# Kernel tuning notes

Measured on AMD Instinct MI355X. Metric: run time of the kernel, lower is better.

## Reference

```python
import jax, jax.numpy as jnp
import numpy as np

B, S, D = 4, 4096, 1024
GROUP = 256
HEAD = 128
INNER = 2048


def setup_inputs() -> dict:
    key = jax.random.key(0)
    ks = jax.random.split(key, 16)
    s = 0.02
    return {
        'x': jax.random.normal(ks[0], (B, S, D), jnp.float32),
        'Wv': jax.random.normal(ks[1], (D, INNER), jnp.float32) * s,
        'bv': jnp.zeros((INNER,), jnp.float32),
        'Wg': jax.random.normal(ks[2], (D, INNER), jnp.float32) * s,
        'bg': jnp.zeros((INNER,), jnp.float32),
        'Win': jax.random.normal(ks[3], (D, HEAD), jnp.float32) * s,
        'bin_': jnp.zeros((HEAD,), jnp.float32),
        'Wout': jax.random.normal(ks[4], (INNER, D), jnp.float32) * s,
        'bout': jnp.zeros((D,), jnp.float32),
        'g_qq': 1.0 + jax.random.normal(ks[5], (HEAD,), jnp.float32) * s,
        'b_qq': jnp.zeros((HEAD,), jnp.float32),
        'g_qk': 1.0 + jax.random.normal(ks[6], (HEAD,), jnp.float32) * s,
        'b_qk': jnp.zeros((HEAD,), jnp.float32),
        'g_lq': 1.0 + jax.random.normal(ks[7], (HEAD,), jnp.float32) * s,
        'b_lq': jnp.zeros((HEAD,), jnp.float32),
        'g_lk': 1.0 + jax.random.normal(ks[8], (HEAD,), jnp.float32) * s,
        'b_lk': jnp.zeros((HEAD,), jnp.float32),
    }


def reference(x, Wv, bv, Wg, bg, Win, bin_, Wout, bout,
              g_qq, b_qq, g_qk, b_qk, g_lq, b_lq, g_lk, b_lk):
    b, s, d = x.shape
    g = s // GROUP
    xc = x.reshape(b, g, GROUP, d)                       # [B,G,C,D]
    v = jax.nn.silu(xc @ Wv + bv)                        # [B,G,C,E]
    gate = jax.nn.silu(xc @ Wg + bg)                     # [B,G,C,E]
    x_ = jax.nn.silu(xc @ Win + bin_)                    # [B,G,C,H]
    quad_q = x_ * g_qq + b_qq
    quad_k = x_ * g_qk + b_qk
    lin_q = x_ * g_lq + b_lq
    lin_k = x_ * g_lk + b_lk
    # local quadratic relu^2 attention per chunk
    scale = jnp.asarray(INNER ** 0.5, x.dtype)           # v.size(-1)**0.5
    attn = jnp.einsum('bgns,bgms->bgnm', quad_q, quad_k) / scale
    causal_mask = jnp.triu(jnp.ones((GROUP, GROUP), bool), 1)
    attn = jnp.where(causal_mask, 0.0, attn)
    attn = jnp.square(jax.nn.relu(attn))
    v_quad = jnp.einsum('bgnm,bgme->bgne', attn, v)
    # global causal linear attention: exclusive cumsum of per-chunk k^T v over chunks
    kv = jnp.einsum('bgcs,bgce->bgse', lin_k, v)         # [B,G,H,E]
    kv = jnp.cumsum(kv, axis=1) - kv                     # exclusive over chunk dim
    v_lin = jnp.einsum('bgcs,bgse->bgce', lin_q, kv)
    o = (v_quad + v_lin) * gate
    o = o @ Wout + bout
    return o.reshape(b, s, d)
```

## Files before the change

kernel.cpp:

```cpp
#include <hip/hip_runtime.h>

typedef __attribute__((ext_vector_type(8))) short short8;
typedef __attribute__((ext_vector_type(4))) float floatx4;
typedef __attribute__((ext_vector_type(4))) unsigned short ushort4v;
typedef unsigned short u16;

#define DEV __device__ __forceinline__

DEV u16 f2bf(float f) {
  unsigned int u = __float_as_uint(f);
  u += 0x7fffu + ((u >> 16) & 1u);
  return (u16)(u >> 16);
}
DEV float bf2f(u16 h) { return __uint_as_float(((unsigned int)h) << 16); }
DEV float silu_f(float x) { return x / (1.f + __expf(-x)); }
DEV floatx4 fzero() { floatx4 z = {0.f, 0.f, 0.f, 0.f}; return z; }
DEV floatx4 mfma16(short8 a, short8 b, floatx4 c) {
  return __builtin_amdgcn_mfma_f32_16x16x32_bf16(a, b, c, 0, 0, 0);
}
DEV void gll16(const void* g, void* l) {
  __builtin_amdgcn_global_load_lds((__attribute__((address_space(1))) void*)g,
                                   (__attribute__((address_space(3))) void*)l,
                                   16, 0, 0);
}

__global__ __launch_bounds__(256) void cast_x_kernel(const float* __restrict__ x,
                                                     u16* __restrict__ xb, int n4) {
  int i = blockIdx.x * 256 + threadIdx.x;
  if (i >= n4) return;
  float4 v = ((const float4*)x)[i];
  ushort4v o;
  o[0] = f2bf(v.x); o[1] = f2bf(v.y); o[2] = f2bf(v.z); o[3] = f2bf(v.w);
  *(ushort4v*)&xb[(size_t)i * 4] = o;
}

__global__ __launch_bounds__(256) void transpose_cast_kernel(const float* __restrict__ W,
                                                             u16* __restrict__ WT,
                                                             int K, int N) {
  __shared__ u16 tile[32][36];
  int n0 = blockIdx.x * 32, k0 = blockIdx.y * 32;
  int t = threadIdx.x;
  int r = t >> 3, cs = (t & 7) * 4;
  float4 v = *(const float4*)&W[(size_t)(k0 + r) * N + n0 + cs];
  tile[r][cs + 0] = f2bf(v.x);
  tile[r][cs + 1] = f2bf(v.y);
  tile[r][cs + 2] = f2bf(v.z);
  tile[r][cs + 3] = f2bf(v.w);
  __syncthreads();
  ushort4v o;
  o[0] = tile[cs + 0][r];
  o[1] = tile[cs + 1][r];
  o[2] = tile[cs + 2][r];
  o[3] = tile[cs + 3][r];
  *(ushort4v*)&WT[(size_t)(n0 + r) * K + k0 + cs] = o;
}

DEV void wave_transposed_store(u16* __restrict__ Ct, long chunk_stride,
                               const u16* trw, int chunk, int cbase, int nbase,
                               int lane) {
#pragma unroll
  for (int it = 0; it < 8; ++it) {
    int e_l = it * 8 + (lane >> 3);
    int c_off = (lane & 7) * 8;
    short8 val = *(const short8*)&trw[e_l * 72 + c_off];
    *(short8*)&Ct[(size_t)chunk * chunk_stride + (size_t)(nbase + e_l) * 256 + cbase +
                  c_off] = val;
  }
}


#define PH(SA, SB, NIA, NIB, VML, RDA, STG, HH)                                \
  {                                                                            \
    asm volatile("s_waitcnt vmcnt(" #VML ")" ::: "memory");                    \
    if (RDA) {                                                                 \
      _Pragma("unroll") for (int mi_ = 0; mi_ < 8; ++mi_)                      \
          af[mi_] = *(const short8*)&lds[((SA) * 1024 + aoff + mi_ * 64) * 8]; \
    }                                                                          \
    bf0 = *(const short8*)&lds[((SB) * 1024 + boff + (NIA) * 64) * 8];         \
    bf1 = *(const short8*)&lds[((SB) * 1024 + boff + (NIB) * 64) * 8];         \
    if (STG) STAGE(HH);                                                        \
    asm volatile("" ::: "memory");                                             \
    __builtin_amdgcn_s_barrier();                                              \
    asm volatile("" ::: "memory");                                             \
    __builtin_amdgcn_s_setprio(1);                                             \
    _Pragma("unroll") for (int mi_ = 0; mi_ < 8; ++mi_) {                      \
      acc[mi_][NIA] = mfma16(af[mi_], bf0, acc[mi_][NIA]);                     \
      acc[mi_][NIB] = mfma16(af[mi_], bf1, acc[mi_][NIB]);                     \
    }                                                                          \
    __builtin_amdgcn_s_setprio(0);                                             \
    asm volatile("" ::: "memory");                                             \
    __builtin_amdgcn_s_barrier();                                              \
    asm volatile("" ::: "memory");                                             \
  }

template <int MODE>
__global__ __launch_bounds__(512, 2) void gemm8(
    const u16* __restrict__ A, const u16* __restrict__ Bt,
    const float* __restrict__ bias0, const float* __restrict__ bias1,
    u16* __restrict__ vT, u16* __restrict__ gate, float* __restrict__ Cf) {
  constexpr int KK = (MODE == 0) ? 1024 : 2048;
  constexpr int NN = (MODE == 0) ? 4096 : 1024;
  constexpr int NT = KK / 64;
  constexpr int NSH = (MODE == 0) ? 4 : 2;

  __shared__ u16 lds[8 * 8192];

  const int t = threadIdx.x;
  const int wave = t >> 6, lane = t & 63;
  const int l15 = lane & 15, l16 = lane >> 4;
  const int b = blockIdx.x;
  const int xcd = b & 7, i = b >> 3;
  const int m0 = (xcd * 8 + (i >> NSH)) * 256;
  const int n0 = (i & ((1 << NSH) - 1)) * 256;
  const int wm = wave >> 2, wn = wave & 3;

  const int o0 = wave * 128 + lane;
  const int r0 = o0 >> 2;
  const int p0 = (o0 & 3) ^ ((r0 >> 1) & 3);
  const u16* srcA = A + (size_t)(m0 + r0) * KK + p0 * 8;
  const u16* srcB = Bt + (size_t)(n0 + r0) * KK + p0 * 8;

  auto STAGE = [&](int h) {
    const int slot = h & 7;
    const int koff = (h >> 2) * 64 + ((h >> 1) & 1) * 32;
    u16* dst = &lds[slot * 8192 + o0 * 8];
    const u16* s = ((h & 1) ? srcB : srcA) + koff;
    gll16(s, dst);
    gll16(s + 16 * KK, dst + 512);
  };

  const int rA = wm * 128 + l15;
  const int aoff = rA * 4 + (l16 ^ ((rA >> 1) & 3));
  const int rB = wn * 64 + l15;
  const int boff = rB * 4 + (l16 ^ ((rB >> 1) & 3));

  floatx4 acc[8][4];
#pragma unroll
  for (int a = 0; a < 8; ++a)
#pragma unroll
    for (int c = 0; c < 4; ++c) acc[a][c] = fzero();
  short8 af[8], bf0, bf1;

#pragma unroll
  for (int h = 0; h < 7; ++h) STAGE(h);
  asm volatile("s_waitcnt vmcnt(10)" ::: "memory");
  asm volatile("" ::: "memory");
  __builtin_amdgcn_s_barrier();
  asm volatile("" ::: "memory");

  for (int T = 0; T < NT - 2; ++T) {
    const int s0 = (T & 1) * 4;
    PH(s0, s0 + 1, 0, 1, 8, 1, 1, 4 * T + 7)
    PH(s0, s0 + 1, 2, 3, 8, 0, 1, 4 * T + 8)
    PH(s0 + 2, s0 + 3, 0, 1, 8, 1, 1, 4 * T + 9)
    PH(s0 + 2, s0 + 3, 2, 3, 8, 0, 1, 4 * T + 10)
  }
  {
    const int s0 = ((NT - 2) & 1) * 4;
    PH(s0, s0 + 1, 0, 1, 8, 1, 1, 4 * (NT - 2) + 7)
    PH(s0, s0 + 1, 2, 3, 8, 0, 0, 0)
    PH(s0 + 2, s0 + 3, 0, 1, 6, 1, 0, 0)
    PH(s0 + 2, s0 + 3, 2, 3, 4, 0, 0, 0)
  }
  {
    const int s0 = ((NT - 1) & 1) * 4;
    PH(s0, s0 + 1, 0, 1, 2, 1, 0, 0)
    PH(s0, s0 + 1, 2, 3, 0, 0, 0, 0)
    PH(s0 + 2, s0 + 3, 0, 1, 0, 1, 0, 0)
    PH(s0 + 2, s0 + 3, 2, 3, 0, 0, 0, 0)
  }

  if constexpr (MODE == 0) {
    const int chunk = m0 >> 8;
    u16* trw = &lds[wave * (64 * 72)];
    if (n0 < 2048) {
      const int e0 = n0 + wn * 64;
#pragma unroll
      for (int th = 0; th < 2; ++th) {
#pragma unroll
        for (int mi2 = 0; mi2 < 4; ++mi2) {
          const int mi = th * 4 + mi2;
#pragma unroll
          for (int ni = 0; ni < 4; ++ni) {
            const float bc = bias0[e0 + ni * 16 + l15];
            ushort4v pk;
#pragma unroll
            for (int r = 0; r < 4; ++r) pk[r] = f2bf(silu_f(acc[mi][ni][r] + bc));
            *(ushort4v*)&trw[(ni * 16 + l15) * 72 + mi2 * 16 + l16 * 4] = pk;
          }
        }
        wave_transposed_store(vT, 2048L * 256, trw, chunk, wm * 128 + th * 64, e0,
                              lane);
      }
    } else {
      const int c0 = n0 - 2048 + wn * 64;
#pragma unroll
      for (int th = 0; th < 2; ++th) {
#pragma unroll
        for (int mi2 = 0; mi2 < 4; ++mi2) {
          const int mi = th * 4 + mi2;
#pragma unroll
          for (int ni = 0; ni < 4; ++ni) {
            const float bc = bias1[c0 + ni * 16 + l15];
#pragma unroll
            for (int r = 0; r < 4; ++r)
              trw[(mi2 * 16 + l16 * 4 + r) * 72 + ni * 16 + l15] =
                  f2bf(silu_f(acc[mi][ni][r] + bc));
          }
        }
#pragma unroll
        for (int it = 0; it < 8; ++it) {
          const int m_l = it * 8 + (lane >> 3);
          const int n_off = (lane & 7) * 8;
          *(short8*)&gate[(size_t)(m0 + wm * 128 + th * 64 + m_l) * 2048 + c0 +
                          n_off] = *(const short8*)&trw[m_l * 72 + n_off];
        }
      }
    }
  } else {
#pragma unroll
    for (int mi = 0; mi < 8; ++mi)
#pragma unroll
      for (int ni = 0; ni < 4; ++ni) {
        const int col = n0 + wn * 64 + ni * 16 + l15;
        const float bc = bias0[col];
        const int row = m0 + wm * 128 + mi * 16 + l16 * 4;
#pragma unroll
        for (int r = 0; r < 4; ++r)
          Cf[(size_t)(row + r) * NN + col] = acc[mi][ni][r] + bc;
      }
  }
}

template <int MODE>
__global__ __launch_bounds__(256) void gemm_bt(
    const u16* __restrict__ A, const u16* __restrict__ Bt, int M, int N, int K,
    int nshift, const float* __restrict__ bias, u16* __restrict__ Cn,
    float* __restrict__ Cf, u16* __restrict__ Ct, long ct_stride,
    u16* __restrict__ Cn2, u16* __restrict__ Cn3,
    const float* __restrict__ gqq, const float* __restrict__ bqq,
    const float* __restrict__ gqk, const float* __restrict__ bqk,
    const float* __restrict__ glq, const float* __restrict__ blq,
    const float* __restrict__ glk, const float* __restrict__ blk) {
  __shared__ union {
    struct { u16 a[128 * 64]; u16 b[128 * 64]; } st;
    u16 tr[4 * 64 * 72];
  } sm;
  const int t = threadIdx.x;
  const int wave = t >> 6, lane = t & 63;
  const int l15 = lane & 15, l16 = lane >> 4;
  const int ell = blockIdx.x;
  const int xcd = ell & 7, i = ell >> 3;
  const int mtiles_per_xcd = M >> 10;
  const int m0 = (xcd * mtiles_per_xcd + (i >> nshift)) * 128;
  const int n0 = (i & ((1 << nshift) - 1)) * 128;
  const int wm = (wave >> 1) * 64, wn = (wave & 1) * 64;

  floatx4 acc[4][4];
#pragma unroll
  for (int i2 = 0; i2 < 4; ++i2)
#pragma unroll
    for (int j = 0; j < 4; ++j) acc[i2][j] = fzero();

  const u16* pa[4];
  const u16* pb[4];
#pragma unroll
  for (int j = 0; j < 4; ++j) {
    const int c = t + 256 * j;
    const int r = c >> 3, p = c & 7;
    const int g = p ^ (r & 7);
    pa[j] = A + (size_t)(m0 + r) * K + g * 8;
    pb[j] = Bt + (size_t)(n0 + r) * K + g * 8;
  }

  for (int k0 = 0; k0 < K; k0 += 64) {
    __syncthreads();
#pragma unroll
    for (int j = 0; j < 4; ++j) {
      gll16(pa[j] + k0, &sm.st.a[(t + 256 * j) * 8]);
      gll16(pb[j] + k0, &sm.st.b[(t + 256 * j) * 8]);
    }
    __syncthreads();
#pragma unroll
    for (int s = 0; s < 2; ++s) {
      short8 af[4], bfr[4];
#pragma unroll
      for (int mi = 0; mi < 4; ++mi) {
        const int wr = wm + mi * 16 + l15;
        af[mi] = *(const short8*)&sm.st.a[wr * 64 + ((s * 4 + l16) ^ (wr & 7)) * 8];
      }
#pragma unroll
      for (int ni = 0; ni < 4; ++ni) {
        const int wr = wn + ni * 16 + l15;
        bfr[ni] = *(const short8*)&sm.st.b[wr * 64 + ((s * 4 + l16) ^ (wr & 7)) * 8];
      }
#pragma unroll
      for (int mi = 0; mi < 4; ++mi)
#pragma unroll
        for (int ni = 0; ni < 4; ++ni)
          acc[mi][ni] = mfma16(af[mi], bfr[ni], acc[mi][ni]);
    }
  }
  __syncthreads();

  if constexpr (MODE == 3) {
#pragma unroll
    for (int mi = 0; mi < 4; ++mi)
#pragma unroll
      for (int ni = 0; ni < 4; ++ni) {
        const int col = n0 + wn + ni * 16 + l15;
        const float bc = bias[col];
        const int row = m0 + wm + mi * 16 + l16 * 4;
#pragma unroll
        for (int r = 0; r < 4; ++r)
          Cf[(size_t)(row + r) * N + col] = acc[mi][ni][r] + bc;
      }
  } else {
    u16* trw = &sm.tr[wave * 64 * 72];
#pragma unroll
    for (int mi = 0; mi < 4; ++mi)
#pragma unroll
      for (int ni = 0; ni < 4; ++ni) {
        const int col = wn + ni * 16 + l15;
        const float bc = bias[col];
        const float Gqq = gqq[col], Bqq = bqq[col];
        const float Gqk = gqk[col], Bqk = bqk[col];
        const float Glq = glq[col], Blq = blq[col];
        const float Glk = glk[col], Blk = blk[col];
        const int row = m0 + wm + mi * 16 + l16 * 4;
        ushort4v p;
#pragma unroll
        for (int r = 0; r < 4; ++r) {
          const float sv = silu_f(acc[mi][ni][r] + bc);
          const size_t ad = (size_t)(row + r) * N + col;
          Cn[ad] = f2bf(sv * Gqq + Bqq);
          Cn2[ad] = f2bf(sv * Gqk + Bqk);
          Cn3[ad] = f2bf(sv * Glq + Blq);
          p[r] = f2bf(sv * Glk + Blk);
        }
        *(ushort4v*)&trw[(ni * 16 + l15) * 72 + mi * 16 + l16 * 4] = p;
      }
    wave_transposed_store(Ct, ct_stride, trw, (m0 + wm) >> 8, (m0 + wm) & 255, wn,
                          lane);
  }
}

__global__ __launch_bounds__(256) void kv_kernel(const u16* __restrict__ vT,
                                                 const u16* __restrict__ lkT,
                                                 u16* __restrict__ kv) {
  const int chunk = blockIdx.y;
  const int et = blockIdx.x;
  const int w = threadIdx.x >> 6, lane = threadIdx.x & 63;
  const int l15 = lane & 15, l16 = lane >> 4;
  const size_t vb = (size_t)chunk * (2048 * 256) + (size_t)et * (128 * 256);
  const size_t lb = (size_t)chunk * (128 * 256);
  const int we = (w >> 1) * 64, wh = (w & 1) * 64;
  floatx4 acc[4][4];
#pragma unroll
  for (int i = 0; i < 4; ++i)
#pragma unroll
    for (int j = 0; j < 4; ++j) acc[i][j] = fzero();
  for (int kk = 0; kk < 8; ++kk) {
    short8 av[4], bv[4];
#pragma unroll
    for (int mi = 0; mi < 4; ++mi)
      av[mi] = *(const short8*)&vT[vb + (size_t)(we + mi * 16 + l15) * 256 + kk * 32 +
                                   l16 * 8];
#pragma unroll
    for (int ni = 0; ni < 4; ++ni)
      bv[ni] = *(const short8*)&lkT[lb + (size_t)(wh + ni * 16 + l15) * 256 + kk * 32 +
                                    l16 * 8];
#pragma unroll
    for (int mi = 0; mi < 4; ++mi)
#pragma unroll
      for (int ni = 0; ni < 4; ++ni) acc[mi][ni] = mfma16(av[mi], bv[ni], acc[mi][ni]);
  }
  u16* out = kv + (size_t)chunk * (2048 * 128);
#pragma unroll
  for (int mi = 0; mi < 4; ++mi)
#pragma unroll
    for (int ni = 0; ni < 4; ++ni) {
      const int h = wh + ni * 16 + l15;
      const int e = et * 128 + we + mi * 16 + l16 * 4;
#pragma unroll
      for (int r = 0; r < 4; ++r) out[(size_t)(e + r) * 128 + h] = f2bf(acc[mi][ni][r]);
    }
}

__global__ __launch_bounds__(256) void cumsum_kernel(u16* __restrict__ kv) {
  const int idx = blockIdx.x * 256 + threadIdx.x;
  const int b = blockIdx.y;
  float s = 0.f;
  for (int g = 0; g < 16; ++g) {
    const size_t a = (size_t)(b * 16 + g) * 262144 + idx;
    const float v = bf2f(kv[a]);
    kv[a] = f2bf(s);
    s += v;
  }
}

__global__ __launch_bounds__(256) void attn_kernel(
    const u16* __restrict__ qq, const u16* __restrict__ qk, const u16* __restrict__ lq,
    const u16* __restrict__ vT, const u16* __restrict__ kvT,
    u16* __restrict__ gate_op) {
  __shared__ u16 S[64][264];
  const int chunk = blockIdx.y;
  const int e0 = blockIdx.x * 256;
  const int tok0 = chunk * 256;
  const int w = threadIdx.x >> 6, lane = threadIdx.x & 63;
  const int l15 = lane & 15, l16 = lane >> 4;
  const float isc = 0.022097086912079608f;
  const size_t vbase = (size_t)chunk * (2048 * 256);
  const size_t kbase = (size_t)chunk * (2048 * 128);
  const int ew = e0 + w * 64;

  for (int ns = 0; ns < 4; ++ns) {
    const int r0 = ns * 64 + w * 16;
    short8 af[4];
#pragma unroll
    for (int kk = 0; kk < 4; ++kk)
      af[kk] = *(const short8*)&qq[(size_t)(tok0 + r0 + l15) * 128 + kk * 32 + l16 * 8];
    const int mt_cnt = (r0 >> 4) + 1;
    const int mt_all = (ns + 1) * 4;
    const int srow = w * 16 + l16 * 4;
    for (int mt = 0; mt < mt_all; ++mt) {
      if (mt < mt_cnt) {
        floatx4 a = fzero();
#pragma unroll
        for (int kk = 0; kk < 4; ++kk) {
          short8 bq =
              *(const short8*)&qk[(size_t)(tok0 + mt * 16 + l15) * 128 + kk * 32 +
                                  l16 * 8];
          a = mfma16(af[kk], bq, a);
        }
        const int mcol = mt * 16 + l15;
#pragma unroll
        for (int r = 0; r < 4; ++r) {
          const int nrow = r0 + l16 * 4 + r;
          float sv = a[r] * isc;
          sv = (mcol <= nrow) ? sv : 0.f;
          sv = fmaxf(sv, 0.f);
          S[srow + r][mcol] = f2bf(sv * sv);
        }
      } else {
#pragma unroll
        for (int r = 0; r < 4; ++r) S[srow + r][mt * 16 + l15] = (u16)0;
      }
    }
    __syncthreads();

    floatx4 acc[4][4];
#pragma unroll
    for (int i = 0; i < 4; ++i)
#pragma unroll
      for (int j = 0; j < 4; ++j) acc[i][j] = fzero();

    const int ks = (ns + 1) * 2;
    for (int kk = 0; kk < ks; ++kk) {
      short8 sa[4];
#pragma unroll
      for (int nt = 0; nt < 4; ++nt)
        sa[nt] = *(const short8*)&S[nt * 16 + l15][kk * 32 + l16 * 8];
#pragma unroll
      for (int ei = 0; ei < 4; ++ei) {
        short8 vb = *(const short8*)&vT[vbase + (size_t)(ew + ei * 16 + l15) * 256 +
                                        kk * 32 + l16 * 8];
#pragma unroll
        for (int nt = 0; nt < 4; ++nt) acc[nt][ei] = mfma16(sa[nt], vb, acc[nt][ei]);
      }
    }
#pragma unroll
    for (int kk = 0; kk < 4; ++kk) {
      short8 la[4];
#pragma unroll
      for (int nt = 0; nt < 4; ++nt)
        la[nt] = *(const short8*)&lq[(size_t)(tok0 + ns * 64 + nt * 16 + l15) * 128 +
                                     kk * 32 + l16 * 8];
#pragma unroll
      for (int ei = 0; ei < 4; ++ei) {
        short8 kb = *(const short8*)&kvT[kbase + (size_t)(ew + ei * 16 + l15) * 128 +
                                         kk * 32 + l16 * 8];
#pragma unroll
        for (int nt = 0; nt < 4; ++nt) acc[nt][ei] = mfma16(la[nt], kb, acc[nt][ei]);
      }
    }
#pragma unroll
    for (int nt = 0; nt < 4; ++nt)
#pragma unroll
      for (int ei = 0; ei < 4; ++ei) {
        const int e_g = ew + ei * 16 + l15;
        const int nb = tok0 + ns * 64 + nt * 16 + l16 * 4;
#pragma unroll
        for (int r = 0; r < 4; ++r) {
          const size_t ad = (size_t)(nb + r) * 2048 + e_g;
          const float gv = bf2f(gate_op[ad]);
          gate_op[ad] = f2bf(acc[nt][ei][r] * gv);
        }
      }
    __syncthreads();
  }
}

extern "C" void kernel_launch(void* const* d_in, const int* in_sizes, int n_in,
                              void* d_out, int out_size, void* d_ws, size_t ws_size,
                              hipStream_t stream) {
  (void)in_sizes; (void)n_in; (void)out_size; (void)ws_size;
  const float* x = (const float*)d_in[0];
  const float* Wv = (const float*)d_in[1];
  const float* bv = (const float*)d_in[2];
  const float* Wg = (const float*)d_in[3];
  const float* bg = (const float*)d_in[4];
  const float* Win = (const float*)d_in[5];
  const float* bin = (const float*)d_in[6];
  const float* Wout = (const float*)d_in[7];
  const float* bout = (const float*)d_in[8];
  const float* gqq = (const float*)d_in[9];
  const float* bqq = (const float*)d_in[10];
  const float* gqk = (const float*)d_in[11];
  const float* bqk = (const float*)d_in[12];
  const float* glq = (const float*)d_in[13];
  const float* blq = (const float*)d_in[14];
  const float* glk = (const float*)d_in[15];
  const float* blk = (const float*)d_in[16];

  char* p = (char*)d_ws;
  u16* xb = (u16*)p;   p += (size_t)16384 * 1024 * 2;
  u16* wvT = (u16*)p;  p += (size_t)2048 * 1024 * 2;
  u16* wgT = (u16*)p;  p += (size_t)2048 * 1024 * 2;
  u16* winT = (u16*)p; p += (size_t)128 * 1024 * 2;
  u16* woT = (u16*)p;  p += (size_t)1024 * 2048 * 2;
  u16* vTb = (u16*)p;  p += (size_t)64 * 2048 * 256 * 2;
  u16* gate = (u16*)p; p += (size_t)16384 * 2048 * 2;
  u16* qqb = (u16*)p;  p += (size_t)16384 * 128 * 2;
  u16* qkb = (u16*)p;  p += (size_t)16384 * 128 * 2;
  u16* lqb = (u16*)p;  p += (size_t)16384 * 128 * 2;
  u16* lkTb = (u16*)p; p += (size_t)64 * 128 * 256 * 2;
  u16* kvb = (u16*)p;  p += (size_t)64 * 2048 * 128 * 2;

  cast_x_kernel<<<16384, 256, 0, stream>>>(x, xb, 4194304);
  transpose_cast_kernel<<<dim3(64, 32), 256, 0, stream>>>(Wv, wvT, 1024, 2048);
  transpose_cast_kernel<<<dim3(64, 32), 256, 0, stream>>>(Wg, wgT, 1024, 2048);
  transpose_cast_kernel<<<dim3(4, 32), 256, 0, stream>>>(Win, winT, 1024, 128);
  transpose_cast_kernel<<<dim3(32, 64), 256, 0, stream>>>(Wout, woT, 2048, 1024);

  gemm8<0><<<1024, 512, 0, stream>>>(xb, wvT, bv, bg, vTb, gate, nullptr);

  gemm_bt<2><<<128, 256, 0, stream>>>(
      xb, winT, 16384, 128, 1024, 0, bin, qqb, nullptr, lkTb, 128L * 256, qkb, lqb,
      gqq, bqq, gqk, bqk, glq, blq, glk, blk);

  kv_kernel<<<dim3(16, 64), 256, 0, stream>>>(vTb, lkTb, kvb);
  cumsum_kernel<<<dim3(1024, 4), 256, 0, stream>>>(kvb);
  attn_kernel<<<dim3(8, 64), 256, 0, stream>>>(qqb, qkb, lqb, vTb, kvb, gate);

  gemm8<1><<<256, 512, 0, stream>>>(gate, woT, bout, nullptr, nullptr, nullptr,
                                    (float*)d_out);
}
```

Before: 567.0 us.

## Restructure GEMM main loop into two phases per K-tile with one barrier each

Replaces the four-phase GEMM pipeline (two barriers per phase, half the B fragments per phase) with two phases per K-tile. Each phase issues two stages of global-to-LDS loads, reads all A and B fragments, runs the full 8x4 MFMA block, then hits a single barrier. The prefetch depth drops from 7 to 6 stages and the vmcnt thresholds are adjusted to match. The aim is to halve barrier and synchronisation overhead and give larger uninterrupted MFMA bursts. The cost is less interleaving of LDS reads with MFMAs and slightly shallower load lookahead.

```diff
diff --git a/kernel.cpp b/kernel.cpp
--- a/kernel.cpp
+++ b/kernel.cpp
@@ -69,28 +69,23 @@
 }
 
 
-#define PH(SA, SB, NIA, NIB, VML, RDA, STG, HH)                                \
-  {                                                                            \
-    asm volatile("s_waitcnt vmcnt(" #VML ")" ::: "memory");                    \
-    if (RDA) {                                                                 \
-      _Pragma("unroll") for (int mi_ = 0; mi_ < 8; ++mi_)                      \
-          af[mi_] = *(const short8*)&lds[((SA) * 1024 + aoff + mi_ * 64) * 8]; \
-    }                                                                          \
-    bf0 = *(const short8*)&lds[((SB) * 1024 + boff + (NIA) * 64) * 8];         \
-    bf1 = *(const short8*)&lds[((SB) * 1024 + boff + (NIB) * 64) * 8];         \
-    if (STG) STAGE(HH);                                                        \
-    asm volatile("" ::: "memory");                                             \
-    __builtin_amdgcn_s_barrier();                                              \
-    asm volatile("" ::: "memory");                                             \
-    __builtin_amdgcn_s_setprio(1);                                             \
-    _Pragma("unroll") for (int mi_ = 0; mi_ < 8; ++mi_) {                      \
-      acc[mi_][NIA] = mfma16(af[mi_], bf0, acc[mi_][NIA]);                     \
-      acc[mi_][NIB] = mfma16(af[mi_], bf1, acc[mi_][NIB]);                     \
-    }                                                                          \
-    __builtin_amdgcn_s_setprio(0);                                             \
-    asm volatile("" ::: "memory");                                             \
-    __builtin_amdgcn_s_barrier();                                              \
-    asm volatile("" ::: "memory");                                             \
+#define PH2(SA, SB, VML, STG, HH)                                            \
+  {                                                                          \
+    asm volatile("s_waitcnt vmcnt(" #VML ")" ::: "memory");                  \
+    if (STG) { STAGE(HH); STAGE((HH) + 1); }                                 \
+    _Pragma("unroll") for (int mi_ = 0; mi_ < 8; ++mi_)                      \
+        af[mi_] = *(const short8*)&lds[((SA) * 1024 + aoff + mi_ * 64) * 8]; \
+    _Pragma("unroll") for (int ni_ = 0; ni_ < 4; ++ni_)                      \
+        bf[ni_] = *(const short8*)&lds[((SB) * 1024 + boff + ni_ * 64) * 8]; \
+    asm volatile("" ::: "memory");                                           \
+    __builtin_amdgcn_s_setprio(1);                                           \
+    _Pragma("unroll") for (int mi_ = 0; mi_ < 8; ++mi_)                      \
+      _Pragma("unroll") for (int ni_ = 0; ni_ < 4; ++ni_)                    \
+          acc[mi_][ni_] = mfma16(af[mi_], bf[ni_], acc[mi_][ni_]);           \
+    __builtin_amdgcn_s_setprio(0);                                           \
+    asm volatile("" ::: "memory");                                           \
+    __builtin_amdgcn_s_barrier();                                            \
+    asm volatile("" ::: "memory");                                           \
   }
 
 template <int MODE>
@@ -139,35 +134,29 @@
   for (int a = 0; a < 8; ++a)
 #pragma unroll
     for (int c = 0; c < 4; ++c) acc[a][c] = fzero();
-  short8 af[8], bf0, bf1;
-
-#pragma unroll
-  for (int h = 0; h < 7; ++h) STAGE(h);
-  asm volatile("s_waitcnt vmcnt(10)" ::: "memory");
+  short8 af[8], bf[4];
+
+#pragma unroll
+  for (int h = 0; h < 6; ++h) STAGE(h);
+  asm volatile("s_waitcnt vmcnt(8)" ::: "memory");
   asm volatile("" ::: "memory");
   __builtin_amdgcn_s_barrier();
   asm volatile("" ::: "memory");
 
   for (int T = 0; T < NT - 2; ++T) {
     const int s0 = (T & 1) * 4;
-    PH(s0, s0 + 1, 0, 1, 8, 1, 1, 4 * T + 7)
-    PH(s0, s0 + 1, 2, 3, 8, 0, 1, 4 * T + 8)
-    PH(s0 + 2, s0 + 3, 0, 1, 8, 1, 1, 4 * T + 9)
-    PH(s0 + 2, s0 + 3, 2, 3, 8, 0, 1, 4 * T + 10)
+    PH2(s0, s0 + 1, 4, 1, 4 * T + 6)
+    PH2(s0 + 2, s0 + 3, 4, 1, 4 * T + 8)
   }
   {
     const int s0 = ((NT - 2) & 1) * 4;
-    PH(s0, s0 + 1, 0, 1, 8, 1, 1, 4 * (NT - 2) + 7)
-    PH(s0, s0 + 1, 2, 3, 8, 0, 0, 0)
-    PH(s0 + 2, s0 + 3, 0, 1, 6, 1, 0, 0)
-    PH(s0 + 2, s0 + 3, 2, 3, 4, 0, 0, 0)
+    PH2(s0, s0 + 1, 4, 1, 4 * (NT - 2) + 6)
+    PH2(s0 + 2, s0 + 3, 4, 0, 0)
   }
   {
     const int s0 = ((NT - 1) & 1) * 4;
-    PH(s0, s0 + 1, 0, 1, 2, 1, 0, 0)
-    PH(s0, s0 + 1, 2, 3, 0, 0, 0, 0)
-    PH(s0 + 2, s0 + 3, 0, 1, 0, 1, 0, 0)
-    PH(s0 + 2, s0 + 3, 2, 3, 0, 0, 0, 0)
+    PH2(s0, s0 + 1, 0, 0, 0)
+    PH2(s0 + 2, s0 + 3, 0, 0, 0)
   }
 
   if constexpr (MODE == 0) {
```

Measured after the change: 555.1 us. -2.1%, faster.
